# Kernel optimization log

Measured on AMD Instinct MI355X. Metric: run time of the kernel, lower is better.

Reference implementation:

```python
import jax, jax.numpy as jnp
import numpy as np
from jax import lax

VOCAB, D_EMB, D_HID, N_CLS = 32000, 512, 512, 4
B, T = 32, 2048


def setup_inputs() -> dict:
    key = jax.random.key(0)
    ks = jax.random.split(key, 8)
    s_emb = 1.0 / np.sqrt(D_EMB)
    s_hid = 1.0 / np.sqrt(D_HID)
    return {
        "x": jax.random.randint(ks[0], (B, T), 0, VOCAB, dtype=jnp.int64),
        "attn": jnp.ones((B, T), dtype=jnp.int32),
        "embedding": jax.random.normal(ks[1], (VOCAB, D_EMB), jnp.float32) * s_emb,
        "W_ih": jax.random.uniform(ks[2], (4 * D_HID, D_EMB), jnp.float32, -s_hid, s_hid),
        "W_hh": jax.random.uniform(ks[3], (4 * D_HID, D_HID), jnp.float32, -s_hid, s_hid),
        "b_ih": jax.random.uniform(ks[4], (4 * D_HID,), jnp.float32, -s_hid, s_hid),
        "b_hh": jax.random.uniform(ks[5], (4 * D_HID,), jnp.float32, -s_hid, s_hid),
        "fc_W": jax.random.uniform(ks[6], (N_CLS, D_HID), jnp.float32, -s_hid, s_hid),
        "fc_b": jax.random.uniform(ks[7], (N_CLS,), jnp.float32, -s_hid, s_hid),
    }


def _lstm_forward(x, embedding, W_ih, W_hh, b_ih, b_hh):
    b, t = x.shape
    h_dim = W_hh.shape[1]
    emb = embedding[x]                                  # [B, T, E]
    # input projection for all timesteps at once (same math as per-step cell)
    x_proj = jnp.einsum('bte,ge->tbg', emb, W_ih) + b_ih  # [T, B, 4H]

    def step(carry, xp):
        h, c = carry
        gates = xp + h @ W_hh.T + b_hh                  # [B, 4H]
        i, f, g, o = jnp.split(gates, 4, axis=-1)
        c = jax.nn.sigmoid(f) * c + jax.nn.sigmoid(i) * jnp.tanh(g)
        h = jax.nn.sigmoid(o) * jnp.tanh(c)
        return (h, c), h

    h0 = jnp.zeros((b, h_dim), emb.dtype)
    (_, _), hs = lax.scan(step, (h0, h0), x_proj)       # hs: [T, B, H]
    return hs


def reference(x, attn, embedding, W_ih, W_hh, b_ih, b_hh, fc_W, fc_b):
    hs = _lstm_forward(x, embedding, W_ih, W_hh, b_ih, b_hh)  # [T, B, H]
    lengths = jnp.sum(attn, axis=1).astype(jnp.int32) - 1     # [B]
    last_hs = hs[lengths, jnp.arange(hs.shape[1])]            # [B, H] vectorized gather
    logits = last_hs @ fc_W.T + fc_b                          # [B, n_classes]
    return logits
```

## Files before the change

kernel.cpp:

```cpp
#include <hip/hip_runtime.h>
#include <math.h>

typedef unsigned int u32;

#define T_SEQ   2048
#define NWG     256

#define OFF_HBUF   0
#define OFF_CNT    131072
#define OFF_LASTH  135168
#define WS_NEED    200704ull

#define FB_OFF_HBUF   0
#define FB_OFF_ARRIVE 131072
#define FB_OFF_LASTH  131328

#define DYN_LDS_BYTES 148480

__device__ __forceinline__ float sigm(float x) { return 1.0f / (1.0f + expf(-x)); }

__device__ __forceinline__ float4 ldg4s(const float* p) {
  float4 v;
  asm volatile("global_load_dwordx4 %0, %1, off sc0 sc1" : "=v"(v) : "v"(p) : "memory");
  return v;
}
__device__ __forceinline__ void stg1fs(float* p, float v) {
  asm volatile("global_store_dword %0, %1, off sc0 sc1" :: "v"(p), "v"(v) : "memory");
}

__global__ void __launch_bounds__(256, 1)
lstm_seq(const int* __restrict__ x, const int* __restrict__ attn,
         const float* __restrict__ emb,
         const float* __restrict__ Wih, const float* __restrict__ Whh,
         const float* __restrict__ bih, const float* __restrict__ bhh,
         float* __restrict__ hbuf, u32* __restrict__ counters,
         float* __restrict__ lasth)
{
  extern __shared__ __align__(16) char smem[];
  float4* Wl4 = (float4*)smem;
  float4* Hl4 = (float4*)(smem + 131072);
  float*  gsc = (float*)(smem + 131072 + 16384);
  __shared__ int s_dead;

  const int tid = threadIdx.x, bid = blockIdx.x;
  const int ug = bid >> 2, bg = bid & 3;
  const int wv = tid >> 6, lane = tid & 63;
  const int kg = lane >> 2, inner = lane & 3;
  const int rowg = wv * 2 + (inner >> 1);
  const int bbase = (inner & 1) * 4;

  u32* cntb = counters + bg * 256;
  u32* mycnt = cntb + (ug & 7) * 32;

#pragma unroll
  for (int k = 0; k < 32; ++k) {
    int cf = tid + k * 256;
    int r  = cf >> 8, c = cf & 255;
    int R  = (r >> 3) * 512 + ug * 8 + (r & 7);
    const float* src = (c < 128) ? (Wih + (size_t)R * 512 + c * 4)
                                 : (Whh + (size_t)R * 512 + (c - 128) * 4);
    float4 v = *(const float4*)src;
    int p = r * 256 + (c & ~7) + (((c & 7) + ((c >> 3) & 15) + (r >> 2)) & 7);
    Wl4[p] = v;
  }

  {
    int b = tid & 7, c = tid >> 3;
    const int4* ap = (const int4*)(attn + (size_t)(bg * 8 + b) * 2048 + c * 64);
    int s = 0;
#pragma unroll
    for (int k = 0; k < 16; ++k) { int4 a = ap[k]; s += a.x + a.y + a.z + a.w; }
    gsc[c * 8 + b] = (float)s;
  }
  if (tid == 0) s_dead = 0;
  __syncthreads();
  int len = 0; float c_reg = 0.f;
  float bI = 0, bF = 0, bG = 0, bO = 0;
  if (tid < 64) {
    int b = tid & 7, uu = tid >> 3;
    int s = 0;
#pragma unroll
    for (int c = 0; c < 32; ++c) s += (int)gsc[c * 8 + b];
    len = s - 1; if (len < 0) len = T_SEQ - 1;
    int gu = ug * 8 + uu;
    bI = bih[gu]        + bhh[gu];
    bF = bih[512 + gu]  + bhh[512 + gu];
    bG = bih[1024 + gu] + bhh[1024 + gu];
    bO = bih[1536 + gu] + bhh[1536 + gu];
  }
  __syncthreads();

  bool dead = false;
  float4 w[4][8];

  for (int t = 0; t < T_SEQ; ++t) {
    float acc[4][4];
#pragma unroll
    for (int i = 0; i < 4; ++i) { acc[i][0] = 0.f; acc[i][1] = 0.f; acc[i][2] = 0.f; acc[i][3] = 0.f; }

#pragma unroll
    for (int i = 0; i < 4; ++i) {
      int r = rowg * 4 + i;
#pragma unroll
      for (int q = 0; q < 8; ++q)
        w[i][q] = Wl4[r * 256 + kg * 8 + ((q + kg + rowg) & 7)];
    }

#pragma unroll
    for (int jb = 0; jb < 2; ++jb) {
      int xr = x[(size_t)(bg * 8 + bbase + jb) * 2048 + t];
      const float4* ep = (const float4*)(emb + (size_t)xr * 512 + kg * 32);
      float4 e[8];
#pragma unroll
      for (int q = 0; q < 8; ++q) e[q] = ep[q];
#pragma unroll
      for (int q = 0; q < 8; ++q)
#pragma unroll
        for (int i = 0; i < 4; ++i) {
          acc[i][jb] += w[i][q].x * e[q].x; acc[i][jb] += w[i][q].y * e[q].y;
          acc[i][jb] += w[i][q].z * e[q].z; acc[i][jb] += w[i][q].w * e[q].w;
        }
    }

    if (tid < 8 && !dead) {
      const u32 target = (u32)(t << 3);
      const u32* myc = cntb + tid * 32;
      int it = 0;
      while (true) {
        u32 v = __hip_atomic_load(myc, __ATOMIC_RELAXED, __HIP_MEMORY_SCOPE_AGENT);
        if (__all((int)v >= (int)target)) break;
        if (++it > (1 << 16)) { s_dead = 1; break; }
        __builtin_amdgcn_s_sleep(1);
      }
    }
    __syncthreads();
    if (s_dead) dead = true;

    float4 hv[4];
    int pp[4];
    {
      const float* hsrc = hbuf + (((t + 1) & 1) << 14) + (size_t)(bg * 8) * 512;
#pragma unroll
      for (int k = 0; k < 4; ++k) {
        int cf = tid + k * 256;
        int b = cf >> 7, c = cf & 127;
        hv[k] = ldg4s(hsrc + (size_t)b * 512 + c * 4);
        pp[k] = b * 128 + (c & ~7) + (((c & 7) + (c >> 3) + b) & 7);
      }
    }

#pragma unroll
    for (int jb = 2; jb < 4; ++jb) {
      int xr = x[(size_t)(bg * 8 + bbase + jb) * 2048 + t];
      const float4* ep = (const float4*)(emb + (size_t)xr * 512 + kg * 32);
      float4 e[8];
#pragma unroll
      for (int q = 0; q < 8; ++q) e[q] = ep[q];
#pragma unroll
      for (int q = 0; q < 8; ++q)
#pragma unroll
        for (int i = 0; i < 4; ++i) {
          acc[i][jb] += w[i][q].x * e[q].x; acc[i][jb] += w[i][q].y * e[q].y;
          acc[i][jb] += w[i][q].z * e[q].z; acc[i][jb] += w[i][q].w * e[q].w;
        }
    }

    asm volatile("s_waitcnt vmcnt(0)" ::: "memory");
    __builtin_amdgcn_sched_barrier(0);
#pragma unroll
    for (int k = 0; k < 4; ++k) Hl4[pp[k]] = hv[k];
    __syncthreads();

#pragma unroll
    for (int i = 0; i < 4; ++i) {
      int r = rowg * 4 + i;
#pragma unroll
      for (int q = 0; q < 8; ++q)
        w[i][q] = Wl4[r * 256 + 128 + kg * 8 + ((q + kg + rowg) & 7)];
    }
#pragma unroll
    for (int jb = 0; jb < 4; ++jb) {
      int bl = bbase + jb;
      float4 e[8];
#pragma unroll
      for (int q = 0; q < 8; ++q)
        e[q] = Hl4[bl * 128 + kg * 8 + ((q + kg + bl) & 7)];
#pragma unroll
      for (int q = 0; q < 8; ++q)
#pragma unroll
        for (int i = 0; i < 4; ++i) {
          acc[i][jb] += w[i][q].x * e[q].x; acc[i][jb] += w[i][q].y * e[q].y;
          acc[i][jb] += w[i][q].z * e[q].z; acc[i][jb] += w[i][q].w * e[q].w;
        }
    }

#pragma unroll
    for (int i = 0; i < 4; ++i)
#pragma unroll
      for (int j = 0; j < 4; ++j) {
        float v = acc[i][j];
        v += __shfl_xor(v, 4, 64);
        v += __shfl_xor(v, 8, 64);
        v += __shfl_xor(v, 16, 64);
        v += __shfl_xor(v, 32, 64);
        acc[i][j] = v;
      }
    if (lane < 16) {
      int kgl = lane >> 2;
      int r = rowg * 4 + kgl;
#pragma unroll
      for (int j = 0; j < 4; ++j)
        gsc[r * 8 + bbase + j] = acc[kgl][j];
    }
    __syncthreads();

    if (tid < 64) {
      int b = tid & 7, uu = tid >> 3;
      float gi = gsc[(0 * 8 + uu) * 8 + b] + bI;
      float gf = gsc[(1 * 8 + uu) * 8 + b] + bF;
      float gg = gsc[(2 * 8 + uu) * 8 + b] + bG;
      float go = gsc[(3 * 8 + uu) * 8 + b] + bO;
      float iv = sigm(gi), fv = sigm(gf), ov = sigm(go), gv = tanhf(gg);
      c_reg = fv * c_reg + iv * gv;
      float hval = ov * tanhf(c_reg);
      int bglob = bg * 8 + b, unit = ug * 8 + uu;
      float* hd = hbuf + ((t & 1) << 14) + (bglob << 9) + unit;
      stg1fs(hd, hval);
      if (t == len) lasth[(bglob << 9) + unit] = hval;
      asm volatile("s_waitcnt vmcnt(0)" ::: "memory");
      if (tid == 0)
        __hip_atomic_fetch_add(mycnt, 1u, __ATOMIC_RELAXED, __HIP_MEMORY_SCOPE_AGENT);
    }
  }
}

__global__ void __launch_bounds__(128)
fc_kernel(const float* __restrict__ lasth, const float* __restrict__ fcW,
          const float* __restrict__ fcb, float* __restrict__ out)
{
  int tid = threadIdx.x;
  int b = tid >> 2, n = tid & 3;
  const float4* h4 = (const float4*)(lasth + (size_t)b * 512);
  const float4* w4 = (const float4*)(fcW + (size_t)n * 512);
  float s0 = 0.f, s1 = 0.f, s2 = 0.f, s3 = 0.f;
#pragma unroll 8
  for (int k = 0; k < 128; ++k) {
    float4 a = h4[k], c = w4[k];
    s0 += a.x * c.x; s1 += a.y * c.y; s2 += a.z * c.z; s3 += a.w * c.w;
  }
  out[b * 4 + n] = fcb[n] + ((s0 + s1) + (s2 + s3));
}

__device__ __forceinline__ void gl2lds16(const void* gsrc, void* ldst) {
  __builtin_amdgcn_global_load_lds(
      (const __attribute__((address_space(1))) u32*)gsrc,
      (__attribute__((address_space(3))) u32*)ldst, 16, 0, 0);
}

__global__ void __launch_bounds__(256)
lstm_persist(const int* __restrict__ xidx, const int* __restrict__ attn,
             const float* __restrict__ emb,
             const float* __restrict__ Wih, const float* __restrict__ Whh,
             const float* __restrict__ bih, const float* __restrict__ bhh,
             float* __restrict__ hbuf, float* __restrict__ lasth,
             u32* __restrict__ arrive)
{
  __shared__ __align__(16) float Wl[8][1024];
  __shared__ __align__(16) float ul[2][32][64];
  __shared__ float gsc[32][8];

  const int tid  = threadIdx.x;
  const int wg   = blockIdx.x;
  const int lane = tid & 63;
  const int wv   = tid >> 6;
  const int r    = tid & 7;
  const int bb   = tid >> 3;
  const int brl  = bb & 7;

#pragma unroll 2
  for (int i = 0; i < 8; ++i) {
    int ci = i * 256 + tid;
    int rr = ci >> 8;
    int cc = ci & 255;
    int R  = ((rr >> 1) << 9) + (wg * 2 + (rr & 1));
    const float* src = (cc < 128) ? (Wih + (size_t)R * 512 + cc * 4)
                                  : (Whh + (size_t)R * 512 + (cc - 128) * 4);
    float4 v = *(const float4*)src;
    int slot = cc ^ (rr & 7);
    *(float4*)&Wl[rr][slot * 4] = v;
  }
  float bias;
  {
    int R = ((r >> 1) << 9) + (wg * 2 + (r & 1));
    bias = bih[R] + bhh[R];
  }
  {
    int pb = tid >> 3, pc = tid & 7;
    const int4* ap = (const int4*)(attn + pb * 2048 + pc * 256);
    int s = 0;
#pragma unroll 8
    for (int k = 0; k < 64; ++k) { int4 a = ap[k]; s += a.x + a.y + a.z + a.w; }
    gsc[pb][pc] = (float)s;
  }
  __syncthreads();
  int   len_reg = 0;
  float c_reg   = 0.f;
  if (tid < 64) {
    int b2 = tid & 31;
    int s = 0;
#pragma unroll
    for (int k = 0; k < 8; ++k) s += (int)gsc[b2][k];
    len_reg = s - 1;
    if (len_reg < 0) len_reg = 2047;
  }
  __syncthreads();

  const int idx_b = 8 * wv + (lane & 7);
  int idx_cur = xidx[(size_t)idx_b * 2048];

  for (int t = 0; t < T_SEQ; ++t) {
    int idx_next = (t < T_SEQ - 1) ? xidx[(size_t)idx_b * 2048 + t + 1] : 0;
    float a0 = bias, a1 = 0.f, a2 = 0.f, a3 = 0.f;
    const float* hsrc = hbuf + (((t + 1) & 1) << 14);

    auto stageE = [&](int jt, int buf) {
#pragma unroll
      for (int q = 0; q < 2; ++q) {
        int rlq = 4 * q + (lane >> 4);
        int sc = lane & 15;
        int kc = sc ^ (rlq & 7);
        int rowg = __shfl(idx_cur, rlq, 64);
        const float* g = emb + (size_t)rowg * 512 + jt * 64 + kc * 4;
        gl2lds16(g, (void*)&ul[buf][8 * wv + 4 * q][0]);
      }
    };
    auto stageH = [&](int jt, int buf) {
#pragma unroll
      for (int q = 0; q < 2; ++q) {
        int rlq = 4 * q + (lane >> 4);
        int sc = lane & 15;
        int kc = sc ^ (rlq & 7);
        int blq = 8 * wv + rlq;
        const float* g = hsrc + (size_t)blq * 512 + jt * 64 + kc * 4;
        gl2lds16(g, (void*)&ul[buf][8 * wv + 4 * q][0]);
      }
    };
    auto computeT = [&](int jg, int buf) {
#pragma unroll
      for (int kc = 0; kc < 16; ++kc) {
        float4 uv4 = *(const float4*)&ul[buf][bb][(kc ^ brl) * 4];
        float4 wv4 = *(const float4*)&Wl[r][(((jg << 4) + kc) ^ r) * 4];
        a0 += uv4.x * wv4.x; a1 += uv4.y * wv4.y;
        a2 += uv4.z * wv4.z; a3 += uv4.w * wv4.w;
      }
    };

    stageE(0, 0);
#pragma unroll
    for (int jt = 0; jt < 8; ++jt) {
      if (jt < 7) { stageE(jt + 1, (jt + 1) & 1); asm volatile("s_waitcnt vmcnt(2)" ::: "memory"); }
      else       { asm volatile("s_waitcnt vmcnt(0)" ::: "memory"); }
      computeT(jt, jt & 1);
    }

    if (tid == 0) {
      u32 target = (u32)t << 8;
      while (__hip_atomic_load(arrive, __ATOMIC_RELAXED, __HIP_MEMORY_SCOPE_AGENT) < target)
        __builtin_amdgcn_s_sleep(2);
    }
    __syncthreads();
    __builtin_amdgcn_fence(__ATOMIC_ACQUIRE, "agent");

    stageH(0, 0);
#pragma unroll
    for (int jt = 0; jt < 8; ++jt) {
      if (jt < 7) { stageH(jt + 1, (jt + 1) & 1); asm volatile("s_waitcnt vmcnt(2)" ::: "memory"); }
      else       { asm volatile("s_waitcnt vmcnt(0)" ::: "memory"); }
      computeT(8 + jt, jt & 1);
    }

    gsc[bb][r] = a0 + a1 + a2 + a3;
    __syncthreads();
    if (tid < 64) {
      int u  = tid >> 5;
      int b2 = tid & 31;
      float gi = gsc[b2][u];
      float gf = gsc[b2][2 + u];
      float gg = gsc[b2][4 + u];
      float go = gsc[b2][6 + u];
      float iv = sigm(gi), fv = sigm(gf), ov = sigm(go);
      float gv = tanhf(gg);
      c_reg = fv * c_reg + iv * gv;
      float hv = ov * tanhf(c_reg);
      int unit = (wg << 1) + u;
      hbuf[((t & 1) << 14) + (b2 << 9) + unit] = hv;
      if (t == len_reg) lasth[(b2 << 9) + unit] = hv;
      __builtin_amdgcn_fence(__ATOMIC_RELEASE, "agent");
      if (tid == 0)
        __hip_atomic_fetch_add(arrive, 1u, __ATOMIC_RELAXED, __HIP_MEMORY_SCOPE_AGENT);
    }
    idx_cur = idx_next;
  }
}

extern "C" void kernel_launch(void* const* d_in, const int* in_sizes, int n_in,
                              void* d_out, int out_size, void* d_ws, size_t ws_size,
                              hipStream_t stream) {
  const int*   x    = (const int*)d_in[0];
  const int*   attn = (const int*)d_in[1];
  const float* emb  = (const float*)d_in[2];
  const float* Wih  = (const float*)d_in[3];
  const float* Whh  = (const float*)d_in[4];
  const float* bih  = (const float*)d_in[5];
  const float* bhh  = (const float*)d_in[6];
  const float* fcW  = (const float*)d_in[7];
  const float* fcb  = (const float*)d_in[8];
  float* out = (float*)d_out;
  char* ws = (char*)d_ws;

  if (ws_size >= WS_NEED) {
    float* hbuf  = (float*)(ws + OFF_HBUF);
    u32*   cnts  = (u32*)(ws + OFF_CNT);
    float* lasth = (float*)(ws + OFF_LASTH);

    (void)hipFuncSetAttribute((const void*)lstm_seq,
                              hipFuncAttributeMaxDynamicSharedMemorySize, DYN_LDS_BYTES);
    (void)hipMemsetAsync(ws, 0, OFF_LASTH, stream);

    hipLaunchKernelGGL(lstm_seq, dim3(NWG), dim3(256), DYN_LDS_BYTES, stream,
                       x, attn, emb, Wih, Whh, bih, bhh, hbuf, cnts, lasth);
    hipLaunchKernelGGL(fc_kernel, dim3(1), dim3(128), 0, stream,
                       lasth, fcW, fcb, out);
  } else {
    float* hbuf   = (float*)(ws + FB_OFF_HBUF);
    u32*   arrive = (u32*)(ws + FB_OFF_ARRIVE);
    float* lasth  = (float*)(ws + FB_OFF_LASTH);
    (void)hipMemsetAsync(ws, 0, 131072 + 256, stream);
    hipLaunchKernelGGL(lstm_persist, dim3(256), dim3(256), 0, stream,
                       x, attn, emb, Wih, Whh, bih, bhh, hbuf, lasth, arrive);
    hipLaunchKernelGGL(fc_kernel, dim3(1), dim3(128), 0, stream,
                       lasth, fcW, fcb, out);
  }
}
```

Measured before the change: 14.36 ms.

## Hold LSTM weight slices in registers and double the persistent workgroup count

Each workgroup now owns 4 hidden units instead of 8. The grid doubles to 512 with two workgroups per CU. The W_ih/W_hh slices move from a 145KB dynamic-LDS copy into per-thread registers, so weights are no longer re-read from LDS every timestep. The K dimension is split finer across lanes, which adds one shuffle-reduction stage, and the step barrier now waits for 16 arrivals per counter. This removes per-step LDS weight traffic and spreads the matrix work over more CUs. The costs are much higher register pressure, a grid that relies on all 512 workgroups being co-resident, and more participants in the global spin barrier.

Result: slower. 40.68 ms (+183.3%).

```diff
diff --git a/kernel.cpp b/kernel.cpp
--- a/kernel.cpp
+++ b/kernel.cpp
@@ -4,7 +4,7 @@
 typedef unsigned int u32;
 
 #define T_SEQ   2048
-#define NWG     256
+#define NWG     512
 
 #define OFF_HBUF   0
 #define OFF_CNT    131072
@@ -15,8 +15,6 @@
 #define FB_OFF_ARRIVE 131072
 #define FB_OFF_LASTH  131328
 
-#define DYN_LDS_BYTES 148480
-
 __device__ __forceinline__ float sigm(float x) { return 1.0f / (1.0f + expf(-x)); }
 
 __device__ __forceinline__ float4 ldg4s(const float* p) {
@@ -28,7 +26,7 @@
   asm volatile("global_store_dword %0, %1, off sc0 sc1" :: "v"(p), "v"(v) : "memory");
 }
 
-__global__ void __launch_bounds__(256, 1)
+__global__ void __launch_bounds__(256, 2)
 lstm_seq(const int* __restrict__ x, const int* __restrict__ attn,
          const float* __restrict__ emb,
          const float* __restrict__ Wih, const float* __restrict__ Whh,
@@ -36,32 +34,30 @@
          float* __restrict__ hbuf, u32* __restrict__ counters,
          float* __restrict__ lasth)
 {
-  extern __shared__ __align__(16) char smem[];
-  float4* Wl4 = (float4*)smem;
-  float4* Hl4 = (float4*)(smem + 131072);
-  float*  gsc = (float*)(smem + 131072 + 16384);
+  __shared__ __align__(16) float4 Hl4[1024];
+  __shared__ float gsc[256];
   __shared__ int s_dead;
 
   const int tid = threadIdx.x, bid = blockIdx.x;
   const int ug = bid >> 2, bg = bid & 3;
   const int wv = tid >> 6, lane = tid & 63;
-  const int kg = lane >> 2, inner = lane & 3;
-  const int rowg = wv * 2 + (inner >> 1);
-  const int bbase = (inner & 1) * 4;
-
-  u32* cntb = counters + bg * 256;
+  const int kg  = (lane >> 2) & 15;
+  const int kk  = (lane >> 1) & 1;
+  const int bb0 = (lane & 1) * 4;
+  const int ksf = kg * 32 + kk * 16;
+  const int cb  = kg * 8 + kk * 4;
+
+  u32* cntb  = counters + bg * 256;
   u32* mycnt = cntb + (ug & 7) * 32;
 
-#pragma unroll
-  for (int k = 0; k < 32; ++k) {
-    int cf = tid + k * 256;
-    int r  = cf >> 8, c = cf & 255;
-    int R  = (r >> 3) * 512 + ug * 8 + (r & 7);
-    const float* src = (c < 128) ? (Wih + (size_t)R * 512 + c * 4)
-                                 : (Whh + (size_t)R * 512 + (c - 128) * 4);
-    float4 v = *(const float4*)src;
-    int p = r * 256 + (c & ~7) + (((c & 7) + ((c >> 3) & 15) + (r >> 2)) & 7);
-    Wl4[p] = v;
+  float4 wE[4][4], wH[4][4];
+#pragma unroll
+  for (int i = 0; i < 4; ++i) {
+    int R = wv * 512 + ug * 4 + i;
+    const float4* pE = (const float4*)(Wih + (size_t)R * 512 + ksf);
+    const float4* pH = (const float4*)(Whh + (size_t)R * 512 + ksf);
+#pragma unroll
+    for (int q = 0; q < 4; ++q) { wE[i][q] = pE[q]; wH[i][q] = pH[q]; }
   }
 
   {
@@ -76,13 +72,13 @@
   __syncthreads();
   int len = 0; float c_reg = 0.f;
   float bI = 0, bF = 0, bG = 0, bO = 0;
-  if (tid < 64) {
+  if (tid < 32) {
     int b = tid & 7, uu = tid >> 3;
     int s = 0;
 #pragma unroll
     for (int c = 0; c < 32; ++c) s += (int)gsc[c * 8 + b];
     len = s - 1; if (len < 0) len = T_SEQ - 1;
-    int gu = ug * 8 + uu;
+    int gu = ug * 4 + uu;
     bI = bih[gu]        + bhh[gu];
     bF = bih[512 + gu]  + bhh[512 + gu];
     bG = bih[1024 + gu] + bhh[1024 + gu];
@@ -91,7 +87,6 @@
   __syncthreads();
 
   bool dead = false;
-  float4 w[4][8];
 
   for (int t = 0; t < T_SEQ; ++t) {
     float acc[4][4];
@@ -99,47 +94,39 @@
     for (int i = 0; i < 4; ++i) { acc[i][0] = 0.f; acc[i][1] = 0.f; acc[i][2] = 0.f; acc[i][3] = 0.f; }
 
 #pragma unroll
-    for (int i = 0; i < 4; ++i) {
-      int r = rowg * 4 + i;
-#pragma unroll
-      for (int q = 0; q < 8; ++q)
-        w[i][q] = Wl4[r * 256 + kg * 8 + ((q + kg + rowg) & 7)];
-    }
-
-#pragma unroll
-    for (int jb = 0; jb < 2; ++jb) {
-      int xr = x[(size_t)(bg * 8 + bbase + jb) * 2048 + t];
-      const float4* ep = (const float4*)(emb + (size_t)xr * 512 + kg * 32);
-      float4 e[8];
-#pragma unroll
-      for (int q = 0; q < 8; ++q) e[q] = ep[q];
-#pragma unroll
-      for (int q = 0; q < 8; ++q)
+    for (int jb = 0; jb < 4; ++jb) {
+      int xr = x[(size_t)(bg * 8 + bb0 + jb) * 2048 + t];
+      const float4* ep = (const float4*)(emb + (size_t)xr * 512 + ksf);
+      float4 e[4];
+#pragma unroll
+      for (int q = 0; q < 4; ++q) e[q] = ep[q];
+#pragma unroll
+      for (int q = 0; q < 4; ++q)
 #pragma unroll
         for (int i = 0; i < 4; ++i) {
-          acc[i][jb] += w[i][q].x * e[q].x; acc[i][jb] += w[i][q].y * e[q].y;
-          acc[i][jb] += w[i][q].z * e[q].z; acc[i][jb] += w[i][q].w * e[q].w;
+          acc[i][jb] += wE[i][q].x * e[q].x; acc[i][jb] += wE[i][q].y * e[q].y;
+          acc[i][jb] += wE[i][q].z * e[q].z; acc[i][jb] += wE[i][q].w * e[q].w;
         }
     }
 
     if (tid < 8 && !dead) {
-      const u32 target = (u32)(t << 3);
+      const u32 target = (u32)(t << 4);
       const u32* myc = cntb + tid * 32;
       int it = 0;
       while (true) {
         u32 v = __hip_atomic_load(myc, __ATOMIC_RELAXED, __HIP_MEMORY_SCOPE_AGENT);
         if (__all((int)v >= (int)target)) break;
-        if (++it > (1 << 16)) { s_dead = 1; break; }
+        if (++it > (1 << 17)) { s_dead = 1; break; }
         __builtin_amdgcn_s_sleep(1);
       }
     }
     __syncthreads();
     if (s_dead) dead = true;
 
-    float4 hv[4];
-    int pp[4];
     {
       const float* hsrc = hbuf + (((t + 1) & 1) << 14) + (size_t)(bg * 8) * 512;
+      float4 hv[4];
+      int pp[4];
 #pragma unroll
       for (int k = 0; k < 4; ++k) {
         int cf = tid + k * 256;
@@ -147,50 +134,28 @@
         hv[k] = ldg4s(hsrc + (size_t)b * 512 + c * 4);
         pp[k] = b * 128 + (c & ~7) + (((c & 7) + (c >> 3) + b) & 7);
       }
-    }
-
-#pragma unroll
-    for (int jb = 2; jb < 4; ++jb) {
-      int xr = x[(size_t)(bg * 8 + bbase + jb) * 2048 + t];
-      const float4* ep = (const float4*)(emb + (size_t)xr * 512 + kg * 32);
-      float4 e[8];
-#pragma unroll
-      for (int q = 0; q < 8; ++q) e[q] = ep[q];
-#pragma unroll
-      for (int q = 0; q < 8; ++q)
+      asm volatile("s_waitcnt vmcnt(0)" ::: "memory");
+      __builtin_amdgcn_sched_barrier(0);
+#pragma unroll
+      for (int k = 0; k < 4; ++k) Hl4[pp[k]] = hv[k];
+    }
+    __syncthreads();
+
+#pragma unroll
+    for (int jb = 0; jb < 4; ++jb) {
+      int bl = bb0 + jb;
+      float4 e[4];
+#pragma unroll
+      for (int q = 0; q < 4; ++q) {
+        int c = cb + q;
+        e[q] = Hl4[bl * 128 + (c & ~7) + (((c & 7) + (c >> 3) + bl) & 7)];
+      }
+#pragma unroll
+      for (int q = 0; q < 4; ++q)
 #pragma unroll
         for (int i = 0; i < 4; ++i) {
-          acc[i][jb] += w[i][q].x * e[q].x; acc[i][jb] += w[i][q].y * e[q].y;
-          acc[i][jb] += w[i][q].z * e[q].z; acc[i][jb] += w[i][q].w * e[q].w;
-        }
-    }
-
-    asm volatile("s_waitcnt vmcnt(0)" ::: "memory");
-    __builtin_amdgcn_sched_barrier(0);
-#pragma unroll
-    for (int k = 0; k < 4; ++k) Hl4[pp[k]] = hv[k];
-    __syncthreads();
-
-#pragma unroll
-    for (int i = 0; i < 4; ++i) {
-      int r = rowg * 4 + i;
-#pragma unroll
-      for (int q = 0; q < 8; ++q)
-        w[i][q] = Wl4[r * 256 + 128 + kg * 8 + ((q + kg + rowg) & 7)];
-    }
-#pragma unroll
-    for (int jb = 0; jb < 4; ++jb) {
-      int bl = bbase + jb;
-      float4 e[8];
-#pragma unroll
-      for (int q = 0; q < 8; ++q)
-        e[q] = Hl4[bl * 128 + kg * 8 + ((q + kg + bl) & 7)];
-#pragma unroll
-      for (int q = 0; q < 8; ++q)
-#pragma unroll
-        for (int i = 0; i < 4; ++i) {
-          acc[i][jb] += w[i][q].x * e[q].x; acc[i][jb] += w[i][q].y * e[q].y;
-          acc[i][jb] += w[i][q].z * e[q].z; acc[i][jb] += w[i][q].w * e[q].w;
+          acc[i][jb] += wH[i][q].x * e[q].x; acc[i][jb] += wH[i][q].y * e[q].y;
+          acc[i][jb] += wH[i][q].z * e[q].z; acc[i][jb] += wH[i][q].w * e[q].w;
         }
     }
 
@@ -199,34 +164,37 @@
 #pragma unroll
       for (int j = 0; j < 4; ++j) {
         float v = acc[i][j];
+        v += __shfl_xor(v, 2, 64);
         v += __shfl_xor(v, 4, 64);
         v += __shfl_xor(v, 8, 64);
         v += __shfl_xor(v, 16, 64);
         v += __shfl_xor(v, 32, 64);
         acc[i][j] = v;
       }
-    if (lane < 16) {
-      int kgl = lane >> 2;
-      int r = rowg * 4 + kgl;
-#pragma unroll
-      for (int j = 0; j < 4; ++j)
-        gsc[r * 8 + bbase + j] = acc[kgl][j];
+    if (lane < 2) {
+#pragma unroll
+      for (int i = 0; i < 4; ++i)
+#pragma unroll
+        for (int j = 0; j < 4; ++j)
+          gsc[(wv * 4 + i) * 8 + lane * 4 + j] = acc[i][j];
     }
     __syncthreads();
 
     if (tid < 64) {
-      int b = tid & 7, uu = tid >> 3;
-      float gi = gsc[(0 * 8 + uu) * 8 + b] + bI;
-      float gf = gsc[(1 * 8 + uu) * 8 + b] + bF;
-      float gg = gsc[(2 * 8 + uu) * 8 + b] + bG;
-      float go = gsc[(3 * 8 + uu) * 8 + b] + bO;
-      float iv = sigm(gi), fv = sigm(gf), ov = sigm(go), gv = tanhf(gg);
-      c_reg = fv * c_reg + iv * gv;
-      float hval = ov * tanhf(c_reg);
-      int bglob = bg * 8 + b, unit = ug * 8 + uu;
-      float* hd = hbuf + ((t & 1) << 14) + (bglob << 9) + unit;
-      stg1fs(hd, hval);
-      if (t == len) lasth[(bglob << 9) + unit] = hval;
+      if (tid < 32) {
+        int b = tid & 7, uu = tid >> 3;
+        float gi = gsc[(0  + uu) * 8 + b] + bI;
+        float gf = gsc[(4  + uu) * 8 + b] + bF;
+        float gg = gsc[(8  + uu) * 8 + b] + bG;
+        float go = gsc[(12 + uu) * 8 + b] + bO;
+        float iv = sigm(gi), fv = sigm(gf), ov = sigm(go), gv = tanhf(gg);
+        c_reg = fv * c_reg + iv * gv;
+        float hval = ov * tanhf(c_reg);
+        int bglob = bg * 8 + b, unit = ug * 4 + uu;
+        float* hd = hbuf + ((t & 1) << 14) + (bglob << 9) + unit;
+        stg1fs(hd, hval);
+        if (t == len) lasth[(bglob << 9) + unit] = hval;
+      }
       asm volatile("s_waitcnt vmcnt(0)" ::: "memory");
       if (tid == 0)
         __hip_atomic_fetch_add(mycnt, 1u, __ATOMIC_RELAXED, __HIP_MEMORY_SCOPE_AGENT);
@@ -423,11 +391,9 @@
     u32*   cnts  = (u32*)(ws + OFF_CNT);
     float* lasth = (float*)(ws + OFF_LASTH);
 
-    (void)hipFuncSetAttribute((const void*)lstm_seq,
-                              hipFuncAttributeMaxDynamicSharedMemorySize, DYN_LDS_BYTES);
     (void)hipMemsetAsync(ws, 0, OFF_LASTH, stream);
 
-    hipLaunchKernelGGL(lstm_seq, dim3(NWG), dim3(256), DYN_LDS_BYTES, stream,
+    hipLaunchKernelGGL(lstm_seq, dim3(NWG), dim3(256), 0, stream,
                        x, attn, emb, Wih, Whh, bih, bhh, hbuf, cnts, lasth);
     hipLaunchKernelGGL(fc_kernel, dim3(1), dim3(128), 0, stream,
                        lasth, fcW, fcb, out);
```
